# Performance work log

Measured on AMD Instinct MI355X. Metric: run time of the kernel, lower is better.

## Reference

```python
import jax, jax.numpy as jnp
import numpy as np

KERNEL = 31
GROUPS = 8
EPS = 1e-5


def mha1d(x, Wq, Wk, Wv, rel):
    """Sliding-window multi-head attention (MutliHeadAttention1D).
    x: [b, s, in_f]; Wq/Wk/Wv: [out_f, in_f] (torch Linear layout); rel: [1, out_f, KERNEL].
    Returns (out [b, s, out_f], attn [b, s, GROUPS, KERNEL])."""
    b, s, _ = x.shape
    out_f = Wq.shape[0]
    d = out_f // GROUPS
    pad = (KERNEL - 1) // 2
    xp = jnp.pad(x, ((0, 0), (pad, pad), (0, 0)))
    q = jnp.einsum('bsf,of->bso', x, Wq)          # [b, s, out_f]
    k = jnp.einsum('bsf,of->bso', xp, Wk)         # [b, s+2*pad, out_f]
    v = jnp.einsum('bsf,of->bso', xp, Wv)
    # unfold: window index [s, KERNEL]
    idx = jnp.arange(s)[:, None] + jnp.arange(KERNEL)[None, :]
    kw = jnp.swapaxes(k[:, idx], 2, 3) + rel       # [b, s, out_f, KERNEL]
    vw = jnp.swapaxes(v[:, idx], 2, 3)             # [b, s, out_f, KERNEL]
    kw = kw.reshape(b, s, GROUPS, d, KERNEL)
    vw = vw.reshape(b, s, GROUPS, d, KERNEL)
    qh = q.reshape(b, s, GROUPS, d, 1)
    energy = jnp.sum(qh * kw, axis=-2, keepdims=True)   # [b, s, g, 1, K]
    attn = jax.nn.softmax(energy, axis=-1)               # [b, s, g, 1, K]
    out = jnp.sum(attn * vw, axis=-1).reshape(b, s, out_f)
    return out, attn[:, :, :, 0, :]


def layer_norm(x, g, b):
    mu = jnp.mean(x, axis=-1, keepdims=True)
    var = jnp.mean(jnp.square(x - mu), axis=-1, keepdims=True)
    return (x - mu) / jnp.sqrt(var + EPS) * g + b


def setup_inputs() -> dict:
    key = jax.random.key(0)
    ks = jax.random.split(key, 20)
    in_f, mc, out_f = 229, 48, 88
    d = {}
    d['spec'] = jax.random.normal(ks[0], (8, 8192, in_f), dtype=jnp.float32)
    # onset attention block (in 229 -> 48)
    d['Wq1'] = jax.random.normal(ks[1], (mc, in_f), dtype=jnp.float32) * 0.1
    d['Wk1'] = jax.random.normal(ks[2], (mc, in_f), dtype=jnp.float32) * 0.1
    d['Wv1'] = jax.random.normal(ks[3], (mc, in_f), dtype=jnp.float32) * 0.1
    d['rel1'] = jax.random.normal(ks[4], (1, mc, KERNEL), dtype=jnp.float32)
    d['ln1_g'] = jnp.ones((mc,), jnp.float32)
    d['ln1_b'] = jnp.zeros((mc,), jnp.float32)
    d['Wo'] = jax.random.normal(ks[5], (out_f, mc), dtype=jnp.float32) * 0.1
    d['bo'] = jnp.zeros((out_f,), jnp.float32)
    # frame attention block (in 48+88=136 -> 48)
    in2 = mc + out_f
    d['Wq2'] = jax.random.normal(ks[6], (mc, in2), dtype=jnp.float32) * 0.1
    d['Wk2'] = jax.random.normal(ks[7], (mc, in2), dtype=jnp.float32) * 0.1
    d['Wv2'] = jax.random.normal(ks[8], (mc, in2), dtype=jnp.float32) * 0.1
    d['rel2'] = jax.random.normal(ks[9], (1, mc, KERNEL), dtype=jnp.float32)
    d['ln2_g'] = jnp.ones((mc,), jnp.float32)
    d['ln2_b'] = jnp.zeros((mc,), jnp.float32)
    d['Wf'] = jax.random.normal(ks[10], (out_f, mc), dtype=jnp.float32) * 0.1
    d['bf'] = jnp.zeros((out_f,), jnp.float32)
    return d


def reference(spec, Wq1, Wk1, Wv1, rel1, ln1_g, ln1_b, Wo, bo,
              Wq2, Wk2, Wv2, rel2, ln2_g, ln2_b, Wf, bf):
    x, a = mha1d(spec, Wq1, Wk1, Wv1, rel1)
    x = layer_norm(x, ln1_g, ln1_b)
    onset_pred = jax.nn.sigmoid(jnp.einsum('bsm,om->bso', x, Wo) + bo)
    x = jnp.concatenate((onset_pred, x), axis=-1)
    x, _ = mha1d(x, Wq2, Wk2, Wv2, rel2)
    x = layer_norm(x, ln2_g, ln2_b)
    frame_pred = jax.nn.sigmoid(jnp.einsum('bsm,om->bso', x, Wf) + bf)
    return frame_pred, onset_pred, a
```

## Files before the change

### kernel.cpp

```cpp
#include <hip/hip_runtime.h>
#include <math.h>

namespace {

constexpr int B_   = 8;
constexpr int S_   = 8192;
constexpr int NROW = B_ * S_;
constexpr int MC   = 48;
constexpr int OF   = 88;
constexpr int KW   = 31;
constexpr int F1   = 229;
constexpr int F2   = 136;

typedef __attribute__((ext_vector_type(8))) short bf16x8;
typedef __attribute__((ext_vector_type(4))) float f32x4;

__device__ inline unsigned short f2bf(float v) {
    unsigned u = __float_as_uint(v);
    unsigned r = (u + 0x7FFFu + ((u >> 16) & 1u)) >> 16;
    return (unsigned short)r;
}
__device__ inline float bf2f(unsigned short b) {
    return __uint_as_float((unsigned)b << 16);
}
__device__ inline unsigned pack2(unsigned short a, unsigned short b) {
    return (unsigned)a | ((unsigned)b << 16);
}

__global__ void wprep_kernel(const float* __restrict__ Wq,
                             const float* __restrict__ Wk,
                             const float* __restrict__ Wv,
                             int K, int nch, unsigned short* __restrict__ out) {
    int idx = blockIdx.x * 256 + threadIdx.x;
    int kpad = nch * 32;
    int total = 144 * kpad;
    if (idx >= total) return;
    int oc = idx / kpad;
    int kg = idx - oc * kpad;
    int c  = kg >> 5, kk = kg & 31;
    float val = 0.f;
    if (kg < K) {
        const float* W = (oc < 48) ? Wq : (oc < 96 ? Wk : Wv);
        int ocl = (oc < 48) ? oc : (oc < 96 ? oc - 48 : oc - 96);
        val = W[ocl * K + kg];
    }
    unsigned short h = f2bf(val);
    unsigned short l = f2bf(val - bf2f(h));
    size_t base = (size_t)c * 16384 + (size_t)oc * 56 + kk;
    out[base]        = h;
    out[base + 8192] = l;
}

__global__ void woprep_kernel(const float* __restrict__ W,
                              unsigned short* __restrict__ out) {
    int idx = blockIdx.x * 256 + threadIdx.x;
    if (idx >= 96 * 64) return;
    int n = idx >> 6, k = idx & 63;
    float val = (n < OF && k < MC) ? W[n * MC + k] : 0.f;
    unsigned short h = f2bf(val);
    unsigned short l = f2bf(val - bf2f(h));
    out[idx]        = h;
    out[6144 + idx] = l;
}

template<int K, int NCH>
__global__ __launch_bounds__(256) void proj_mfma(
    const float* __restrict__ x,
    const unsigned short* __restrict__ wbuf,
    float* __restrict__ qo, float* __restrict__ ko, float* __restrict__ vo)
{
    __shared__ __attribute__((aligned(16))) unsigned short Ah[64 * 56];
    __shared__ __attribute__((aligned(16))) unsigned short Al[64 * 56];
    __shared__ __attribute__((aligned(16))) unsigned short Bblk[16384];

    const int tid  = threadIdx.x;
    const int row0 = blockIdx.x * 64;
    const int lane = tid & 63;
    const int wm   = tid >> 6;

    f32x4 acc[9];
    #pragma unroll
    for (int nt = 0; nt < 9; ++nt) acc[nt] = f32x4{0.f, 0.f, 0.f, 0.f};

    const int arow = wm * 16 + (lane & 15);
    const int ak   = (lane >> 4) * 8;

    for (int c = 0; c < NCH; ++c) {
        {
            const uint4* src = (const uint4*)(wbuf + (size_t)c * 16384);
            uint4* dst = (uint4*)Bblk;
            #pragma unroll
            for (int i = 0; i < 8; ++i)
                dst[tid + 256 * i] = src[tid + 256 * i];
        }
        const int kc = c * 32;
        #pragma unroll
        for (int i = 0; i < 4; ++i) {
            int idx = tid + 256 * i;
            int r   = idx >> 4;
            int k2  = (idx & 15) * 2;
            int kg  = kc + k2;
            const float* xr = x + (size_t)(row0 + r) * K;
            float v0 = (kg     < K) ? xr[kg]     : 0.f;
            float v1 = (kg + 1 < K) ? xr[kg + 1] : 0.f;
            unsigned short h0 = f2bf(v0), h1 = f2bf(v1);
            unsigned short l0 = f2bf(v0 - bf2f(h0));
            unsigned short l1 = f2bf(v1 - bf2f(h1));
            *(unsigned*)&Ah[r * 56 + k2] = pack2(h0, h1);
            *(unsigned*)&Al[r * 56 + k2] = pack2(l0, l1);
        }
        __syncthreads();

        bf16x8 ah = *(const bf16x8*)&Ah[arow * 56 + ak];
        bf16x8 al = *(const bf16x8*)&Al[arow * 56 + ak];
        #pragma unroll
        for (int nt = 0; nt < 9; ++nt) {
            int bcol = nt * 16 + (lane & 15);
            bf16x8 bh = *(const bf16x8*)&Bblk[bcol * 56 + ak];
            bf16x8 bl = *(const bf16x8*)&Bblk[8192 + bcol * 56 + ak];
            acc[nt] = __builtin_amdgcn_mfma_f32_16x16x32_bf16(ah, bh, acc[nt], 0, 0, 0);
            acc[nt] = __builtin_amdgcn_mfma_f32_16x16x32_bf16(ah, bl, acc[nt], 0, 0, 0);
            acc[nt] = __builtin_amdgcn_mfma_f32_16x16x32_bf16(al, bh, acc[nt], 0, 0, 0);
        }
        __syncthreads();
    }

    const int orow = row0 + wm * 16 + ((lane >> 4) << 2);
    const int ocol = lane & 15;
    #pragma unroll
    for (int nt = 0; nt < 9; ++nt) {
        float* dst = (nt < 3) ? qo : (nt < 6 ? ko : vo);
        int oc = (nt % 3) * 16 + ocol;
        #pragma unroll
        for (int rg = 0; rg < 4; ++rg)
            dst[(size_t)(orow + rg) * MC + oc] = acc[nt][rg];
    }
}

template<bool FIRST>
__global__ __launch_bounds__(512, 8) void attn_core(
    const float* __restrict__ qb,
    const float* __restrict__ kb,
    const float* __restrict__ vb,
    const float* __restrict__ rel,
    const float* __restrict__ lng,
    const float* __restrict__ lnb,
    float* __restrict__ attn_out,
    float* __restrict__ x2)
{
    __shared__ __attribute__((aligned(16))) float ks[94 * 52];
    __shared__ __attribute__((aligned(16))) float vs[94 * 52];
    __shared__ __attribute__((aligned(16))) float relT[31 * 52];
    __shared__ float lngs[48], lnbs[48];

    const int tid = threadIdx.x;
    const int bid = ((blockIdx.x & 7) << 7) | (blockIdx.x >> 3);
    const int bb  = bid >> 7;
    const int st0 = (bid & 127) * 64;
    const size_t base = (size_t)bb * S_;

    for (int idx = tid; idx < 94 * 12; idx += 512) {
        int rr = idx / 12, c4 = idx - rr * 12;
        int si = st0 - 15 + rr;
        float4 k4 = {0.f, 0.f, 0.f, 0.f}, v4 = {0.f, 0.f, 0.f, 0.f};
        if (si >= 0 && si < S_) {
            k4 = *(const float4*)&kb[(base + si) * MC + c4 * 4];
            v4 = *(const float4*)&vb[(base + si) * MC + c4 * 4];
        }
        *(float4*)&ks[rr * 52 + c4 * 4] = k4;
        *(float4*)&vs[rr * 52 + c4 * 4] = v4;
    }
    for (int idx = tid; idx < MC * KW; idx += 512) {
        int c = idx / KW, j = idx - c * KW;
        relT[j * 52 + c] = rel[idx];
    }
    if (tid < 48) { lngs[tid] = lng[tid]; lnbs[tid] = lnb[tid]; }
    __syncthreads();

    const int rl  = tid >> 3;
    const int g   = tid & 7;
    const int ch0 = g * 6;
    const size_t grow = base + st0 + rl;

    const float* qr = qb + grow * MC + ch0;
    float2 q01 = *(const float2*)(qr);
    float2 q23 = *(const float2*)(qr + 2);
    float2 q45 = *(const float2*)(qr + 4);

    float e[KW];
    #pragma unroll
    for (int j = 0; j < KW; ++j) {
        const float* rp = &relT[j * 52 + ch0];
        float2 r01 = *(const float2*)(rp);
        float2 r23 = *(const float2*)(rp + 2);
        float2 r45 = *(const float2*)(rp + 4);
        e[j] = q01.x * r01.x + q01.y * r01.y + q23.x * r23.x
             + q23.y * r23.y + q45.x * r45.x + q45.y * r45.y;
    }
    float mx = -1e30f;
    #pragma unroll
    for (int j = 0; j < KW; ++j) {
        const float* kp = &ks[(rl + j) * 52 + ch0];
        float2 k01 = *(const float2*)(kp);
        float2 k23 = *(const float2*)(kp + 2);
        float2 k45 = *(const float2*)(kp + 4);
        float s = e[j] + q01.x * k01.x + q01.y * k01.y + q23.x * k23.x
                       + q23.y * k23.y + q45.x * k45.x + q45.y * k45.y;
        e[j] = s;
        mx = fmaxf(mx, s);
    }
    float den = 0.f;
    #pragma unroll
    for (int j = 0; j < KW; ++j) { float t = __expf(e[j] - mx); e[j] = t; den += t; }
    float rden = 1.f / den;

    float o0 = 0.f, o1 = 0.f, o2 = 0.f, o3 = 0.f, o4 = 0.f, o5 = 0.f;
    float* aout = FIRST ? (attn_out + (grow * 8 + g) * KW) : nullptr;
    #pragma unroll
    for (int j = 0; j < KW; ++j) {
        float aw = e[j] * rden;
        if constexpr (FIRST) aout[j] = aw;
        const float* vp = &vs[(rl + j) * 52 + ch0];
        float2 v01 = *(const float2*)(vp);
        float2 v23 = *(const float2*)(vp + 2);
        float2 v45 = *(const float2*)(vp + 4);
        o0 += aw * v01.x; o1 += aw * v01.y; o2 += aw * v23.x;
        o3 += aw * v23.y; o4 += aw * v45.x; o5 += aw * v45.y;
    }

    float sum = o0 + o1 + o2 + o3 + o4 + o5;
    sum += __shfl_xor(sum, 1, 8);
    sum += __shfl_xor(sum, 2, 8);
    sum += __shfl_xor(sum, 4, 8);
    float mu = sum * (1.f / 48.f);
    float d0 = o0 - mu, d1 = o1 - mu, d2 = o2 - mu, d3 = o3 - mu, d4 = o4 - mu, d5 = o5 - mu;
    float vr = d0*d0 + d1*d1 + d2*d2 + d3*d3 + d4*d4 + d5*d5;
    vr += __shfl_xor(vr, 1, 8);
    vr += __shfl_xor(vr, 2, 8);
    vr += __shfl_xor(vr, 4, 8);
    float rstd = rsqrtf(vr * (1.f / 48.f) + 1e-5f);

    float* xp = x2 + grow * F2 + OF + ch0;
    *(float2*)(xp)     = float2{d0 * rstd * lngs[ch0]     + lnbs[ch0],
                                d1 * rstd * lngs[ch0 + 1] + lnbs[ch0 + 1]};
    *(float2*)(xp + 2) = float2{d2 * rstd * lngs[ch0 + 2] + lnbs[ch0 + 2],
                                d3 * rstd * lngs[ch0 + 3] + lnbs[ch0 + 3]};
    *(float2*)(xp + 4) = float2{d4 * rstd * lngs[ch0 + 4] + lnbs[ch0 + 4],
                                d5 * rstd * lngs[ch0 + 5] + lnbs[ch0 + 5]};
}

template<bool FIRST>
__global__ __launch_bounds__(256) void pred_gemm(
    const float* __restrict__ x2,
    const unsigned short* __restrict__ wop,
    const float* __restrict__ bo,
    float* __restrict__ pred,
    float* __restrict__ x2w)
{
    __shared__ __attribute__((aligned(16))) unsigned short yh[64 * 72];
    __shared__ __attribute__((aligned(16))) unsigned short yl[64 * 72];
    __shared__ float bosL[96];

    const int tid  = threadIdx.x;
    const int row0 = blockIdx.x * 64;

    for (int idx = tid; idx < 768; idx += 256) {
        int r = idx / 12, c4 = idx - r * 12;
        float4 v4 = *(const float4*)&x2[(size_t)(row0 + r) * F2 + OF + c4 * 4];
        unsigned short h0 = f2bf(v4.x), h1 = f2bf(v4.y), h2 = f2bf(v4.z), h3 = f2bf(v4.w);
        unsigned short l0 = f2bf(v4.x - bf2f(h0)), l1 = f2bf(v4.y - bf2f(h1));
        unsigned short l2 = f2bf(v4.z - bf2f(h2)), l3 = f2bf(v4.w - bf2f(h3));
        *(uint2*)&yh[r * 72 + c4 * 4] = uint2{pack2(h0, h1), pack2(h2, h3)};
        *(uint2*)&yl[r * 72 + c4 * 4] = uint2{pack2(l0, l1), pack2(l2, l3)};
    }
    for (int idx = tid; idx < 384; idx += 256) {
        int r = idx / 6, u = idx - r * 6;
        *(uint2*)&yh[r * 72 + 48 + u * 4] = uint2{0u, 0u};
        *(uint2*)&yl[r * 72 + 48 + u * 4] = uint2{0u, 0u};
    }
    if (tid < 96) bosL[tid] = (tid < OF) ? bo[tid] : 0.f;
    __syncthreads();

    const int l   = tid & 63;
    const int w   = tid >> 6;
    const int lr  = l & 15;
    const int lk8 = (l >> 4) * 8;

    const int arow = w * 16 + lr;
    bf16x8 ah0 = *(const bf16x8*)&yh[arow * 72 + lk8];
    bf16x8 al0 = *(const bf16x8*)&yl[arow * 72 + lk8];
    bf16x8 ah1 = *(const bf16x8*)&yh[arow * 72 + 32 + lk8];
    bf16x8 al1 = *(const bf16x8*)&yl[arow * 72 + 32 + lk8];

    const int rowo = row0 + w * 16 + ((l >> 4) << 2);
    #pragma unroll
    for (int nt = 0; nt < 6; ++nt) {
        int ncol = nt * 16 + lr;
        bf16x8 bh0 = *(const bf16x8*)&wop[(size_t)ncol * 64 + lk8];
        bf16x8 bl0 = *(const bf16x8*)&wop[6144 + (size_t)ncol * 64 + lk8];
        bf16x8 bh1 = *(const bf16x8*)&wop[(size_t)ncol * 64 + 32 + lk8];
        bf16x8 bl1 = *(const bf16x8*)&wop[6144 + (size_t)ncol * 64 + 32 + lk8];
        f32x4 oacc = f32x4{0.f, 0.f, 0.f, 0.f};
        oacc = __builtin_amdgcn_mfma_f32_16x16x32_bf16(ah0, bh0, oacc, 0, 0, 0);
        oacc = __builtin_amdgcn_mfma_f32_16x16x32_bf16(ah0, bl0, oacc, 0, 0, 0);
        oacc = __builtin_amdgcn_mfma_f32_16x16x32_bf16(al0, bh0, oacc, 0, 0, 0);
        oacc = __builtin_amdgcn_mfma_f32_16x16x32_bf16(ah1, bh1, oacc, 0, 0, 0);
        oacc = __builtin_amdgcn_mfma_f32_16x16x32_bf16(ah1, bl1, oacc, 0, 0, 0);
        oacc = __builtin_amdgcn_mfma_f32_16x16x32_bf16(al1, bh1, oacc, 0, 0, 0);
        if (ncol < OF) {
            float bias = bosL[ncol];
            #pragma unroll
            for (int rg = 0; rg < 4; ++rg) {
                float s  = oacc[rg] + bias;
                float sg = 1.f / (1.f + __expf(-s));
                size_t row = (size_t)(rowo + rg);
                pred[row * OF + ncol] = sg;
                if constexpr (FIRST) x2w[row * F2 + ncol] = sg;
            }
        }
    }
}

}

extern "C" void kernel_launch(void* const* d_in, const int* in_sizes, int n_in,
                              void* d_out, int out_size, void* d_ws, size_t ws_size,
                              hipStream_t stream) {
    const float* spec = (const float*)d_in[0];
    const float* Wq1  = (const float*)d_in[1];
    const float* Wk1  = (const float*)d_in[2];
    const float* Wv1  = (const float*)d_in[3];
    const float* rel1 = (const float*)d_in[4];
    const float* ln1g = (const float*)d_in[5];
    const float* ln1b = (const float*)d_in[6];
    const float* Wo   = (const float*)d_in[7];
    const float* bo   = (const float*)d_in[8];
    const float* Wq2  = (const float*)d_in[9];
    const float* Wk2  = (const float*)d_in[10];
    const float* Wv2  = (const float*)d_in[11];
    const float* rel2 = (const float*)d_in[12];
    const float* ln2g = (const float*)d_in[13];
    const float* ln2b = (const float*)d_in[14];
    const float* Wf   = (const float*)d_in[15];
    const float* bf_  = (const float*)d_in[16];

    float* outf   = (float*)d_out;
    float* frame  = outf;
    float* onset  = outf + (size_t)NROW * OF;
    float* attn_a = outf + (size_t)2 * NROW * OF;

    float* wsf = (float*)d_ws;
    float* q1 = wsf;
    float* k1 = q1 + (size_t)NROW * MC;
    float* v1 = k1 + (size_t)NROW * MC;
    float* x2 = v1 + (size_t)NROW * MC;
    unsigned short* wbuf1 = (unsigned short*)(x2 + (size_t)NROW * F2);
    unsigned short* wbuf2 = wbuf1 + (size_t)8 * 16384;
    unsigned short* woP1  = wbuf2 + (size_t)5 * 16384;
    unsigned short* woP2  = woP1 + 2 * 6144;

    wprep_kernel<<<(144 * 8 * 32 + 255) / 256, 256, 0, stream>>>(Wq1, Wk1, Wv1, F1, 8, wbuf1);
    wprep_kernel<<<(144 * 5 * 32 + 255) / 256, 256, 0, stream>>>(Wq2, Wk2, Wv2, F2, 5, wbuf2);
    woprep_kernel<<<24, 256, 0, stream>>>(Wo, woP1);
    woprep_kernel<<<24, 256, 0, stream>>>(Wf, woP2);

    proj_mfma<F1, 8><<<NROW / 64, 256, 0, stream>>>(spec, wbuf1, q1, k1, v1);
    attn_core<true><<<NROW / 64, 512, 0, stream>>>(q1, k1, v1, rel1, ln1g, ln1b,
                                                   attn_a, x2);
    pred_gemm<true><<<NROW / 64, 256, 0, stream>>>(x2, woP1, bo, onset, x2);
    proj_mfma<F2, 5><<<NROW / 64, 256, 0, stream>>>(x2, wbuf2, q1, k1, v1);
    attn_core<false><<<NROW / 64, 512, 0, stream>>>(q1, k1, v1, rel2, ln2g, ln2b,
                                                    nullptr, x2);
    pred_gemm<false><<<NROW / 64, 256, 0, stream>>>(x2, woP2, bf_, frame, nullptr);
}
```

Before: 203.5 us.

## Fuse output-prediction GEMM and sigmoid into the attention kernel epilogue

The attention kernel now writes its layer-normed output as bf16 hi/lo splits into shared memory, reusing the K buffer, and runs the 48->88 MFMA GEMM plus sigmoid in the same block. This removes the separate pred_gemm launches and the round trip of the normalized activations through global memory. The second stage no longer writes x2 at all. The cost is extra shared-memory reuse with additional barriers and a lower occupancy hint (6 instead of 8).

```diff
diff --git a/kernel.cpp b/kernel.cpp
--- a/kernel.cpp
+++ b/kernel.cpp
@@ -138,20 +138,26 @@
 }
 
 template<bool FIRST>
-__global__ __launch_bounds__(512, 8) void attn_core(
+__global__ __launch_bounds__(512, 6) void attn_kernel(
     const float* __restrict__ qb,
     const float* __restrict__ kb,
     const float* __restrict__ vb,
     const float* __restrict__ rel,
     const float* __restrict__ lng,
     const float* __restrict__ lnb,
+    const unsigned short* __restrict__ wop,
+    const float* __restrict__ bo,
+    float* __restrict__ pred,
     float* __restrict__ attn_out,
     float* __restrict__ x2)
 {
     __shared__ __attribute__((aligned(16))) float ks[94 * 52];
     __shared__ __attribute__((aligned(16))) float vs[94 * 52];
     __shared__ __attribute__((aligned(16))) float relT[31 * 52];
+    __shared__ float bosL[96];
     __shared__ float lngs[48], lnbs[48];
+    unsigned short* lnh = (unsigned short*)ks;
+    unsigned short* lnl = lnh + (64 * 48 + 64);
 
     const int tid = threadIdx.x;
     const int bid = ((blockIdx.x & 7) << 7) | (blockIdx.x >> 3);
@@ -174,7 +180,11 @@
         int c = idx / KW, j = idx - c * KW;
         relT[j * 52 + c] = rel[idx];
     }
-    if (tid < 48) { lngs[tid] = lng[tid]; lnbs[tid] = lnb[tid]; }
+    if (tid < 96) bosL[tid] = (tid < OF) ? bo[tid] : 0.f;
+    if (tid >= 128 && tid < 176) {
+        lngs[tid - 128] = lng[tid - 128];
+        lnbs[tid - 128] = lnb[tid - 128];
+    }
     __syncthreads();
 
     const int rl  = tid >> 3;
@@ -239,63 +249,55 @@
     vr += __shfl_xor(vr, 2, 8);
     vr += __shfl_xor(vr, 4, 8);
     float rstd = rsqrtf(vr * (1.f / 48.f) + 1e-5f);
-
-    float* xp = x2 + grow * F2 + OF + ch0;
-    *(float2*)(xp)     = float2{d0 * rstd * lngs[ch0]     + lnbs[ch0],
-                                d1 * rstd * lngs[ch0 + 1] + lnbs[ch0 + 1]};
-    *(float2*)(xp + 2) = float2{d2 * rstd * lngs[ch0 + 2] + lnbs[ch0 + 2],
-                                d3 * rstd * lngs[ch0 + 3] + lnbs[ch0 + 3]};
-    *(float2*)(xp + 4) = float2{d4 * rstd * lngs[ch0 + 4] + lnbs[ch0 + 4],
-                                d5 * rstd * lngs[ch0 + 5] + lnbs[ch0 + 5]};
-}
-
-template<bool FIRST>
-__global__ __launch_bounds__(256) void pred_gemm(
-    const float* __restrict__ x2,
-    const unsigned short* __restrict__ wop,
-    const float* __restrict__ bo,
-    float* __restrict__ pred,
-    float* __restrict__ x2w)
-{
-    __shared__ __attribute__((aligned(16))) unsigned short yh[64 * 72];
-    __shared__ __attribute__((aligned(16))) unsigned short yl[64 * 72];
-    __shared__ float bosL[96];
-
-    const int tid  = threadIdx.x;
-    const int row0 = blockIdx.x * 64;
-
-    for (int idx = tid; idx < 768; idx += 256) {
-        int r = idx / 12, c4 = idx - r * 12;
-        float4 v4 = *(const float4*)&x2[(size_t)(row0 + r) * F2 + OF + c4 * 4];
-        unsigned short h0 = f2bf(v4.x), h1 = f2bf(v4.y), h2 = f2bf(v4.z), h3 = f2bf(v4.w);
-        unsigned short l0 = f2bf(v4.x - bf2f(h0)), l1 = f2bf(v4.y - bf2f(h1));
-        unsigned short l2 = f2bf(v4.z - bf2f(h2)), l3 = f2bf(v4.w - bf2f(h3));
-        *(uint2*)&yh[r * 72 + c4 * 4] = uint2{pack2(h0, h1), pack2(h2, h3)};
-        *(uint2*)&yl[r * 72 + c4 * 4] = uint2{pack2(l0, l1), pack2(l2, l3)};
-    }
-    for (int idx = tid; idx < 384; idx += 256) {
-        int r = idx / 6, u = idx - r * 6;
-        *(uint2*)&yh[r * 72 + 48 + u * 4] = uint2{0u, 0u};
-        *(uint2*)&yl[r * 72 + 48 + u * 4] = uint2{0u, 0u};
-    }
-    if (tid < 96) bosL[tid] = (tid < OF) ? bo[tid] : 0.f;
+    float y0 = d0 * rstd * lngs[ch0]     + lnbs[ch0];
+    float y1 = d1 * rstd * lngs[ch0 + 1] + lnbs[ch0 + 1];
+    float y2 = d2 * rstd * lngs[ch0 + 2] + lnbs[ch0 + 2];
+    float y3 = d3 * rstd * lngs[ch0 + 3] + lnbs[ch0 + 3];
+    float y4 = d4 * rstd * lngs[ch0 + 4] + lnbs[ch0 + 4];
+    float y5 = d5 * rstd * lngs[ch0 + 5] + lnbs[ch0 + 5];
+
+    if constexpr (FIRST) {
+        float* xp = x2 + grow * F2 + OF + ch0;
+        *(float2*)(xp)     = float2{y0, y1};
+        *(float2*)(xp + 2) = float2{y2, y3};
+        *(float2*)(xp + 4) = float2{y4, y5};
+    }
+
     __syncthreads();
 
-    const int l   = tid & 63;
-    const int w   = tid >> 6;
-    const int lr  = l & 15;
-    const int lk8 = (l >> 4) * 8;
-
-    const int arow = w * 16 + lr;
-    bf16x8 ah0 = *(const bf16x8*)&yh[arow * 72 + lk8];
-    bf16x8 al0 = *(const bf16x8*)&yl[arow * 72 + lk8];
-    bf16x8 ah1 = *(const bf16x8*)&yh[arow * 72 + 32 + lk8];
-    bf16x8 al1 = *(const bf16x8*)&yl[arow * 72 + 32 + lk8];
-
-    const int rowo = row0 + w * 16 + ((l >> 4) << 2);
-    #pragma unroll
-    for (int nt = 0; nt < 6; ++nt) {
-        int ncol = nt * 16 + lr;
+    {
+        unsigned short h0 = f2bf(y0), h1 = f2bf(y1), h2 = f2bf(y2);
+        unsigned short h3 = f2bf(y3), h4 = f2bf(y4), h5 = f2bf(y5);
+        unsigned* ph = (unsigned*)&lnh[rl * 48 + ch0];
+        unsigned* pl = (unsigned*)&lnl[rl * 48 + ch0];
+        ph[0] = pack2(h0, h1); ph[1] = pack2(h2, h3); ph[2] = pack2(h4, h5);
+        pl[0] = pack2(f2bf(y0 - bf2f(h0)), f2bf(y1 - bf2f(h1)));
+        pl[1] = pack2(f2bf(y2 - bf2f(h2)), f2bf(y3 - bf2f(h3)));
+        pl[2] = pack2(f2bf(y4 - bf2f(h4)), f2bf(y5 - bf2f(h5)));
+    }
+    if (tid < 64) {
+        lnh[64 * 48 + tid] = 0;
+        lnl[64 * 48 + tid] = 0;
+    }
+    __syncthreads();
+
+    const int l    = tid & 63;
+    const int w    = tid >> 6;
+    const int m    = w & 3;
+    const int ngrp = w >> 2;
+    const int lr   = l & 15;
+    const int lk8  = (l >> 4) * 8;
+
+    const int arow = m * 16 + lr;
+    bf16x8 ah0 = *(const bf16x8*)&lnh[arow * 48 + lk8];
+    bf16x8 al0 = *(const bf16x8*)&lnl[arow * 48 + lk8];
+    bf16x8 ah1 = *(const bf16x8*)&lnh[arow * 48 + 32 + lk8];
+    bf16x8 al1 = *(const bf16x8*)&lnl[arow * 48 + 32 + lk8];
+
+    const int rowo = st0 + m * 16 + ((l >> 4) << 2);
+    #pragma unroll
+    for (int nt = 0; nt < 3; ++nt) {
+        int ncol = (ngrp * 3 + nt) * 16 + lr;
         bf16x8 bh0 = *(const bf16x8*)&wop[(size_t)ncol * 64 + lk8];
         bf16x8 bl0 = *(const bf16x8*)&wop[6144 + (size_t)ncol * 64 + lk8];
         bf16x8 bh1 = *(const bf16x8*)&wop[(size_t)ncol * 64 + 32 + lk8];
@@ -313,9 +315,9 @@
             for (int rg = 0; rg < 4; ++rg) {
                 float s  = oacc[rg] + bias;
                 float sg = 1.f / (1.f + __expf(-s));
-                size_t row = (size_t)(rowo + rg);
+                size_t row = base + rowo + rg;
                 pred[row * OF + ncol] = sg;
-                if constexpr (FIRST) x2w[row * F2 + ncol] = sg;
+                if constexpr (FIRST) x2[row * F2 + ncol] = sg;
             }
         }
     }
@@ -365,11 +367,9 @@
     woprep_kernel<<<24, 256, 0, stream>>>(Wf, woP2);
 
     proj_mfma<F1, 8><<<NROW / 64, 256, 0, stream>>>(spec, wbuf1, q1, k1, v1);
-    attn_core<true><<<NROW / 64, 512, 0, stream>>>(q1, k1, v1, rel1, ln1g, ln1b,
-                                                   attn_a, x2);
-    pred_gemm<true><<<NROW / 64, 256, 0, stream>>>(x2, woP1, bo, onset, x2);
+    attn_kernel<true><<<NROW / 64, 512, 0, stream>>>(q1, k1, v1, rel1, ln1g, ln1b,
+                                                     woP1, bo, onset, attn_a, x2);
     proj_mfma<F2, 5><<<NROW / 64, 256, 0, stream>>>(x2, wbuf2, q1, k1, v1);
-    attn_core<false><<<NROW / 64, 512, 0, stream>>>(q1, k1, v1, rel2, ln2g, ln2b,
-                                                    nullptr, x2);
-    pred_gemm<false><<<NROW / 64, 256, 0, stream>>>(x2, woP2, bf_, frame, nullptr);
-}
+    attn_kernel<false><<<NROW / 64, 512, 0, stream>>>(q1, k1, v1, rel2, ln2g, ln2b,
+                                                      woP2, bf_, frame, nullptr, nullptr);
+}
```

Result: faster. 193.4 us (-5.0%).
